# Performance work log

Measured on AMD Instinct MI355X. Metric: run time of the kernel, lower is better.

Reference implementation:

```python
import jax, jax.numpy as jnp
import numpy as np

HOPS = 3  # max_hops; C has HOPS+1 embedding tables


def setup_inputs() -> dict:
    key = jax.random.key(0)
    k1, k2 = jax.random.split(key)
    # story: [memory_len, batch, token_size]
    story = jax.random.randint(k1, (2048, 64, 4), 0, 50000, dtype=jnp.int64)
    # stacked embedding tables C_0..C_3: [hop+1, vocab, embed_dim], N(0, 0.1)
    C = 0.1 * jax.random.normal(k2, (HOPS + 1, 50000, 128), dtype=jnp.float32)
    return {"story": story, "C": C}


def reference(story, C):
    # story: [M, B, T] -> [B, M, T]
    story = jnp.transpose(story, (1, 0, 2))
    B, M, T = story.shape
    D = C.shape[-1]
    # padding_idx=0 semantics: embedding of token 0 is zero (fwd and bwd)
    pad_mask = (story != 0).astype(C.dtype)[..., None]  # [B, M, T, 1]

    u = jnp.zeros((B, D), dtype=C.dtype)
    for hop in range(HOPS):
        # gather + mask + sum over token dim -> memory keys m_A: [B, M, D]
        m_A = jnp.sum(C[hop][story] * pad_mask, axis=2)
        # attention scores over memory slots, softmax along M
        prob = jax.nn.softmax(jnp.einsum('bmd,bd->bm', m_A, u), axis=1)
        # memory values m_C from next-hop table: [B, M, D]
        m_C = jnp.sum(C[hop + 1][story] * pad_mask, axis=2)
        o_k = jnp.einsum('bm,bmd->bd', prob, m_C)
        u = u + o_k
    return u
```

## Files before the change

kernel.cpp:

```cpp
#include <hip/hip_runtime.h>

#define MM 2048
#define BB 64
#define TT 4
#define DD 128
#define VV 50000
#define VPAD 50176
#define NPART 392
#define NATT 512

typedef float f4v __attribute__((ext_vector_type(4)));
typedef short s8v __attribute__((ext_vector_type(8)));

__device__ __forceinline__ unsigned short f2bf(float f) {
    unsigned int u = __float_as_uint(f);
    u = u + 0x7FFFu + ((u >> 16) & 1u);
    return (unsigned short)(u >> 16);
}
__device__ __forceinline__ float bf2f(unsigned short s) {
    return __uint_as_float((unsigned)s << 16);
}
__device__ __forceinline__ unsigned pk2(float lo, float hi) {
    return ((unsigned)f2bf(hi) << 16) | f2bf(lo);
}

__global__ void k_init(float4* __restrict__ p) {
    p[blockIdx.x * 256 + threadIdx.x] = make_float4(0.f, 0.f, 0.f, 0.f);
}

__global__ __launch_bounds__(256) void k_scatter0(const int* __restrict__ st,
                                                  float* __restrict__ W) {
    const int g = blockIdx.x * 256 + threadIdx.x;
    const int b = g & 63;
    const float p = 1.0f / (float)MM;
    const int4 tk = *(const int4*)(st + (size_t)g * 4);
    if (tk.x) atomicAdd(W + (size_t)tk.x * 64 + b, p);
    if (tk.y) atomicAdd(W + (size_t)tk.y * 64 + b, p);
    if (tk.z) atomicAdd(W + (size_t)tk.z * 64 + b, p);
    if (tk.w) atomicAdd(W + (size_t)tk.w * 64 + b, p);
}

__global__ __launch_bounds__(256, 3) void k_gemm_p(const float* __restrict__ Ch,
                                                   const float* __restrict__ u,
                                                   float* __restrict__ P) {
    __shared__ short lds[192 * 136];
    const int t = threadIdx.x;
    const int v0 = blockIdx.x * 128;

#pragma unroll
    for (int i = 0; i < 24; ++i) {
        const int G = i * 256 + t;
        const int row = G >> 5;
        const int c4 = G & 31;
        float4 val;
        if (row < 128) {
            const int v = v0 + row;
            val = (v < VV) ? *(const float4*)(Ch + (size_t)v * DD + c4 * 4)
                           : make_float4(0.f, 0.f, 0.f, 0.f);
        } else {
            val = *(const float4*)(u + (size_t)(row - 128) * DD + c4 * 4);
        }
        const unsigned int lo = ((unsigned int)f2bf(val.y) << 16) | f2bf(val.x);
        const unsigned int hi = ((unsigned int)f2bf(val.w) << 16) | f2bf(val.z);
        *(uint2*)(lds + row * 136 + c4 * 4) = make_uint2(lo, hi);
    }
    __syncthreads();

    const int l = t & 63;
    const int w = t >> 6;
    const int quad = l >> 4;
    const int n16 = l & 15;

    const int ar0 = (32 * w + n16) * 136;
    const int ar1 = (32 * w + 16 + n16) * 136;
    const int br0 = (128 + n16) * 136;
    const int br1 = (144 + n16) * 136;
    const int br2 = (160 + n16) * 136;
    const int br3 = (176 + n16) * 136;

    f4v c00 = {0.f, 0.f, 0.f, 0.f}, c01 = c00, c02 = c00, c03 = c00;
    f4v c10 = c00, c11 = c00, c12 = c00, c13 = c00;

#pragma unroll
    for (int s = 0; s < 4; ++s) {
        const int ko = s * 32 + quad * 8;
        const s8v a0 = *(const s8v*)(lds + ar0 + ko);
        const s8v a1 = *(const s8v*)(lds + ar1 + ko);
        const s8v b0 = *(const s8v*)(lds + br0 + ko);
        const s8v b1 = *(const s8v*)(lds + br1 + ko);
        const s8v b2 = *(const s8v*)(lds + br2 + ko);
        const s8v b3 = *(const s8v*)(lds + br3 + ko);
        c00 = __builtin_amdgcn_mfma_f32_16x16x32_bf16(a0, b0, c00, 0, 0, 0);
        c01 = __builtin_amdgcn_mfma_f32_16x16x32_bf16(a0, b1, c01, 0, 0, 0);
        c02 = __builtin_amdgcn_mfma_f32_16x16x32_bf16(a0, b2, c02, 0, 0, 0);
        c03 = __builtin_amdgcn_mfma_f32_16x16x32_bf16(a0, b3, c03, 0, 0, 0);
        c10 = __builtin_amdgcn_mfma_f32_16x16x32_bf16(a1, b0, c10, 0, 0, 0);
        c11 = __builtin_amdgcn_mfma_f32_16x16x32_bf16(a1, b1, c11, 0, 0, 0);
        c12 = __builtin_amdgcn_mfma_f32_16x16x32_bf16(a1, b2, c12, 0, 0, 0);
        c13 = __builtin_amdgcn_mfma_f32_16x16x32_bf16(a1, b3, c13, 0, 0, 0);
    }

    const int vb0 = v0 + 32 * w + quad * 4;
    const int vb1 = vb0 + 16;
#pragma unroll
    for (int r = 0; r < 4; ++r) {
        float* __restrict__ P0 = P + (size_t)(vb0 + r) * 64 + n16;
        P0[0] = c00[r]; P0[16] = c01[r]; P0[32] = c02[r]; P0[48] = c03[r];
        float* __restrict__ P1 = P + (size_t)(vb1 + r) * 64 + n16;
        P1[0] = c10[r]; P1[16] = c11[r]; P1[32] = c12[r]; P1[48] = c13[r];
    }
}

__global__ __launch_bounds__(256) void k_attn2(const int* __restrict__ st,
                                               const float* __restrict__ P,
                                               float* __restrict__ W,
                                               float* __restrict__ Zp) {
    __shared__ float eb[256];
    const int tid = threadIdx.x;
    const int g = blockIdx.x * 256 + tid;
    const int b = g & 63;

    const int4 tk = *(const int4*)(st + (size_t)g * 4);
    float s = 0.f;
    if (tk.x) s += P[(size_t)tk.x * 64 + b];
    if (tk.y) s += P[(size_t)tk.y * 64 + b];
    if (tk.z) s += P[(size_t)tk.z * 64 + b];
    if (tk.w) s += P[(size_t)tk.w * 64 + b];
    const float e = __expf(s);
    eb[tid] = e;

    if (tk.x) atomicAdd(W + (size_t)tk.x * 64 + b, e);
    if (tk.y) atomicAdd(W + (size_t)tk.y * 64 + b, e);
    if (tk.z) atomicAdd(W + (size_t)tk.z * 64 + b, e);
    if (tk.w) atomicAdd(W + (size_t)tk.w * 64 + b, e);

    __syncthreads();
    if (tid < 64)
        Zp[(size_t)blockIdx.x * 64 + tid] =
            (eb[tid] + eb[tid + 64]) + (eb[tid + 128] + eb[tid + 192]);
}

__global__ __launch_bounds__(256, 3) void k_gemm_o(const float* __restrict__ C2,
                                                   float* __restrict__ W,
                                                   unsigned* __restrict__ upk,
                                                   const int rezero) {
    __shared__ unsigned Wt[64 * 68];
    __shared__ unsigned Ct[128 * 68];
    const int t = threadIdx.x;
    const int vb = blockIdx.x * 128;

#pragma unroll
    for (int i = 0; i < 4; ++i) {
        const int item = i * 256 + t;
        const int q = item & 15;
        const int p = item >> 4;
        float* w0 = W + (size_t)(vb + 2 * p) * 64 + 4 * q;
        float* w1 = W + (size_t)(vb + 2 * p + 1) * 64 + 4 * q;
        const float4 x = *(const float4*)w0;
        const float4 y = *(const float4*)w1;
        if (rezero) {
            *(float4*)w0 = make_float4(0.f, 0.f, 0.f, 0.f);
            *(float4*)w1 = make_float4(0.f, 0.f, 0.f, 0.f);
        }
        Wt[(4 * q + 0) * 68 + p] = pk2(x.x, y.x);
        Wt[(4 * q + 1) * 68 + p] = pk2(x.y, y.y);
        Wt[(4 * q + 2) * 68 + p] = pk2(x.z, y.z);
        Wt[(4 * q + 3) * 68 + p] = pk2(x.w, y.w);
    }
#pragma unroll
    for (int i = 0; i < 8; ++i) {
        const int item = i * 256 + t;
        const int q = item & 31;
        const int p = item >> 5;
        const int v0 = vb + 2 * p;
        const float4 x = (v0 < VV)
            ? *(const float4*)(C2 + (size_t)v0 * DD + 4 * q)
            : make_float4(0.f, 0.f, 0.f, 0.f);
        const float4 y = (v0 + 1 < VV)
            ? *(const float4*)(C2 + (size_t)(v0 + 1) * DD + 4 * q)
            : make_float4(0.f, 0.f, 0.f, 0.f);
        Ct[(4 * q + 0) * 68 + p] = pk2(x.x, y.x);
        Ct[(4 * q + 1) * 68 + p] = pk2(x.y, y.y);
        Ct[(4 * q + 2) * 68 + p] = pk2(x.z, y.z);
        Ct[(4 * q + 3) * 68 + p] = pk2(x.w, y.w);
    }
    __syncthreads();

    const int l = t & 63;
    const int w = t >> 6;
    const int quad = l >> 4;
    const int n16 = l & 15;

    f4v a00 = {0.f, 0.f, 0.f, 0.f}, a01 = a00;
    f4v a10 = a00, a11 = a00, a20 = a00, a21 = a00, a30 = a00, a31 = a00;

#pragma unroll
    for (int ch = 0; ch < 4; ++ch) {
        const int ku = ch * 16 + quad * 4;
        const s8v wa0 = *(const s8v*)&Wt[(0  + n16) * 68 + ku];
        const s8v wa1 = *(const s8v*)&Wt[(16 + n16) * 68 + ku];
        const s8v wa2 = *(const s8v*)&Wt[(32 + n16) * 68 + ku];
        const s8v wa3 = *(const s8v*)&Wt[(48 + n16) * 68 + ku];
        const s8v cb0 = *(const s8v*)&Ct[(w * 32 + n16) * 68 + ku];
        const s8v cb1 = *(const s8v*)&Ct[(w * 32 + 16 + n16) * 68 + ku];
        a00 = __builtin_amdgcn_mfma_f32_16x16x32_bf16(wa0, cb0, a00, 0, 0, 0);
        a01 = __builtin_amdgcn_mfma_f32_16x16x32_bf16(wa0, cb1, a01, 0, 0, 0);
        a10 = __builtin_amdgcn_mfma_f32_16x16x32_bf16(wa1, cb0, a10, 0, 0, 0);
        a11 = __builtin_amdgcn_mfma_f32_16x16x32_bf16(wa1, cb1, a11, 0, 0, 0);
        a20 = __builtin_amdgcn_mfma_f32_16x16x32_bf16(wa2, cb0, a20, 0, 0, 0);
        a21 = __builtin_amdgcn_mfma_f32_16x16x32_bf16(wa2, cb1, a21, 0, 0, 0);
        a30 = __builtin_amdgcn_mfma_f32_16x16x32_bf16(wa3, cb0, a30, 0, 0, 0);
        a31 = __builtin_amdgcn_mfma_f32_16x16x32_bf16(wa3, cb1, a31, 0, 0, 0);
    }

    unsigned* __restrict__ up = upk + (size_t)blockIdx.x * (BB * 64);
    const int wi = w * 16 + n16;
#pragma unroll
    for (int r = 0; r < 4; ++r) {
        const int br = quad * 4 + r;
        up[(br +  0) * 64 + wi] = pk2(a00[r], a01[r]);
        up[(br + 16) * 64 + wi] = pk2(a10[r], a11[r]);
        up[(br + 32) * 64 + wi] = pk2(a20[r], a21[r]);
        up[(br + 48) * 64 + wi] = pk2(a30[r], a31[r]);
    }
}

__device__ __forceinline__ float zwave(const float* __restrict__ Zp, int b, int tid) {
    const int lane = tid & 63;
    float z = 0.f;
#pragma unroll
    for (int i = 0; i < 8; ++i)
        z += Zp[(size_t)(lane * 8 + i) * 64 + b];
#pragma unroll
    for (int off = 32; off; off >>= 1) z += __shfl_xor(z, off, 64);
    return z;
}

__global__ __launch_bounds__(256) void k_reduce_a(const unsigned* __restrict__ upk,
                                                  float* __restrict__ u) {
    const int jc = blockIdx.x & 15;
    const int kc = blockIdx.x >> 4;
    const int jw = jc * 256 + threadIdx.x;
    const unsigned* __restrict__ p = upk + (size_t)kc * 49 * (BB * 64) + jw;
    float lo = 0.f, hi = 0.f;
#pragma unroll 7
    for (int k = 0; k < 49; ++k) {
        const unsigned w = p[(size_t)k * (BB * 64)];
        lo += bf2f((unsigned short)w);
        hi += bf2f((unsigned short)(w >> 16));
    }
    const int b = jw >> 6, wi = jw & 63;
    const int d0 = (wi >> 4) * 32 + (wi & 15);
    atomicAdd(u + b * DD + d0, lo);
    atomicAdd(u + b * DD + d0 + 16, hi);
}

__global__ __launch_bounds__(256) void k_reduce_az(const unsigned* __restrict__ upk,
                                                   const float* __restrict__ Zp,
                                                   float* __restrict__ u) {
    const int jc = blockIdx.x & 15;
    const int kc = blockIdx.x >> 4;
    const int tid = threadIdx.x;
    const int jw = jc * 256 + tid;
    const int b = jw >> 6;
    const float rz = 1.f / zwave(Zp, b, tid);
    const unsigned* __restrict__ p = upk + (size_t)kc * 49 * (BB * 64) + jw;
    float lo = 0.f, hi = 0.f;
#pragma unroll 7
    for (int k = 0; k < 49; ++k) {
        const unsigned w = p[(size_t)k * (BB * 64)];
        lo += bf2f((unsigned short)w);
        hi += bf2f((unsigned short)(w >> 16));
    }
    const int wi = jw & 63;
    const int d0 = (wi >> 4) * 32 + (wi & 15);
    atomicAdd(u + b * DD + d0, lo * rz);
    atomicAdd(u + b * DD + d0 + 16, hi * rz);
}

__global__ __launch_bounds__(256) void k_reduce_finz(const unsigned* __restrict__ upk,
                                                     const float* __restrict__ Zp,
                                                     const float* __restrict__ u,
                                                     float* __restrict__ out) {
    const int tid = threadIdx.x;
    const int jw = blockIdx.x * 256 + tid;
    const int b = jw >> 6;
    const float rz = 1.f / zwave(Zp, b, tid);
    const unsigned* __restrict__ p = upk + jw;
    float lo = 0.f, hi = 0.f;
#pragma unroll 8
    for (int k = 0; k < NPART; ++k) {
        const unsigned w = p[(size_t)k * (BB * 64)];
        lo += bf2f((unsigned short)w);
        hi += bf2f((unsigned short)(w >> 16));
    }
    const int wi = jw & 63;
    const int d0 = (wi >> 4) * 32 + (wi & 15);
    out[b * DD + d0]      = u[b * DD + d0]      + lo * rz;
    out[b * DD + d0 + 16] = u[b * DD + d0 + 16] + hi * rz;
}

extern "C" void kernel_launch(void* const* d_in, const int* in_sizes, int n_in,
                              void* d_out, int out_size, void* d_ws, size_t ws_size,
                              hipStream_t stream) {
    const int* st = (const int*)d_in[0];
    const float* C = (const float*)d_in[1];

    float* u  = (float*)d_ws;
    float* W  = u + BB * DD;
    float* P  = W + (size_t)VPAD * BB;
    unsigned* upk = (unsigned*)(P + (size_t)VPAD * BB);
    float* Zp = (float*)(upk + (size_t)NPART * BB * 64);

    k_init<<<(BB * DD + VPAD * BB) / 1024, 256, 0, stream>>>((float4*)u);

    k_scatter0<<<(MM * BB) / 256, 256, 0, stream>>>(st, W);
    k_gemm_o<<<VPAD / 128, 256, 0, stream>>>(C + (size_t)1 * VV * DD, W, upk, 1);
    k_reduce_a<<<128, 256, 0, stream>>>(upk, u);

    k_gemm_p<<<VPAD / 128, 256, 0, stream>>>(C + (size_t)1 * VV * DD, u, P);
    k_attn2<<<NATT, 256, 0, stream>>>(st, P, W, Zp);
    k_gemm_o<<<VPAD / 128, 256, 0, stream>>>(C + (size_t)2 * VV * DD, W, upk, 1);
    k_reduce_az<<<128, 256, 0, stream>>>(upk, Zp, u);

    k_gemm_p<<<VPAD / 128, 256, 0, stream>>>(C + (size_t)2 * VV * DD, u, P);
    k_attn2<<<NATT, 256, 0, stream>>>(st, P, W, Zp);
    k_gemm_o<<<VPAD / 128, 256, 0, stream>>>(C + (size_t)3 * VV * DD, W, upk, 0);
    k_reduce_finz<<<16, 256, 0, stream>>>(upk, Zp, u, (float*)d_out);
}
```

Before: 312.6 us.

## Store projection scores in bf16 and use one thread per token in scatter/attention

The per-vocab score table P is now written as bf16 by the projection GEMM and read as bf16 in the attention kernel, halving its footprint and traffic. The scatter and attention kernels now use one thread per token instead of per (slot,batch). Token scores are combined with lane shuffles, and the partial-sum buffer grows to match the larger grid. The goal is more memory-level parallelism for the random gathers and atomics. The cost is bf16 rounding of the scores before exp, plus a longer Z reduction loop.

```diff
diff --git a/kernel.cpp b/kernel.cpp
--- a/kernel.cpp
+++ b/kernel.cpp
@@ -7,7 +7,7 @@
 #define VV 50000
 #define VPAD 50176
 #define NPART 392
-#define NATT 512
+#define NATT 2048
 
 typedef float f4v __attribute__((ext_vector_type(4)));
 typedef short s8v __attribute__((ext_vector_type(8)));
@@ -30,19 +30,15 @@
 
 __global__ __launch_bounds__(256) void k_scatter0(const int* __restrict__ st,
                                                   float* __restrict__ W) {
-    const int g = blockIdx.x * 256 + threadIdx.x;
-    const int b = g & 63;
-    const float p = 1.0f / (float)MM;
-    const int4 tk = *(const int4*)(st + (size_t)g * 4);
-    if (tk.x) atomicAdd(W + (size_t)tk.x * 64 + b, p);
-    if (tk.y) atomicAdd(W + (size_t)tk.y * 64 + b, p);
-    if (tk.z) atomicAdd(W + (size_t)tk.z * 64 + b, p);
-    if (tk.w) atomicAdd(W + (size_t)tk.w * 64 + b, p);
+    const int g4 = blockIdx.x * 256 + threadIdx.x;
+    const int b = (g4 >> 2) & 63;
+    const int tok = st[g4];
+    if (tok) atomicAdd(W + (size_t)tok * 64 + b, 1.0f / (float)MM);
 }
 
 __global__ __launch_bounds__(256, 3) void k_gemm_p(const float* __restrict__ Ch,
                                                    const float* __restrict__ u,
-                                                   float* __restrict__ P) {
+                                                   unsigned short* __restrict__ P16) {
     __shared__ short lds[192 * 136];
     const int t = threadIdx.x;
     const int v0 = blockIdx.x * 128;
@@ -104,40 +100,36 @@
     const int vb1 = vb0 + 16;
 #pragma unroll
     for (int r = 0; r < 4; ++r) {
-        float* __restrict__ P0 = P + (size_t)(vb0 + r) * 64 + n16;
-        P0[0] = c00[r]; P0[16] = c01[r]; P0[32] = c02[r]; P0[48] = c03[r];
-        float* __restrict__ P1 = P + (size_t)(vb1 + r) * 64 + n16;
-        P1[0] = c10[r]; P1[16] = c11[r]; P1[32] = c12[r]; P1[48] = c13[r];
+        unsigned short* __restrict__ P0 = P16 + (size_t)(vb0 + r) * 64 + n16;
+        P0[0]  = f2bf(c00[r]); P0[16] = f2bf(c01[r]);
+        P0[32] = f2bf(c02[r]); P0[48] = f2bf(c03[r]);
+        unsigned short* __restrict__ P1 = P16 + (size_t)(vb1 + r) * 64 + n16;
+        P1[0]  = f2bf(c10[r]); P1[16] = f2bf(c11[r]);
+        P1[32] = f2bf(c12[r]); P1[48] = f2bf(c13[r]);
     }
 }
 
 __global__ __launch_bounds__(256) void k_attn2(const int* __restrict__ st,
-                                               const float* __restrict__ P,
+                                               const unsigned short* __restrict__ P16,
                                                float* __restrict__ W,
                                                float* __restrict__ Zp) {
-    __shared__ float eb[256];
+    __shared__ float eb[64];
     const int tid = threadIdx.x;
-    const int g = blockIdx.x * 256 + tid;
-    const int b = g & 63;
-
-    const int4 tk = *(const int4*)(st + (size_t)g * 4);
-    float s = 0.f;
-    if (tk.x) s += P[(size_t)tk.x * 64 + b];
-    if (tk.y) s += P[(size_t)tk.y * 64 + b];
-    if (tk.z) s += P[(size_t)tk.z * 64 + b];
-    if (tk.w) s += P[(size_t)tk.w * 64 + b];
-    const float e = __expf(s);
-    eb[tid] = e;
-
-    if (tk.x) atomicAdd(W + (size_t)tk.x * 64 + b, e);
-    if (tk.y) atomicAdd(W + (size_t)tk.y * 64 + b, e);
-    if (tk.z) atomicAdd(W + (size_t)tk.z * 64 + b, e);
-    if (tk.w) atomicAdd(W + (size_t)tk.w * 64 + b, e);
-
+    const int g4 = blockIdx.x * 256 + tid;
+    const int b = (g4 >> 2) & 63;
+
+    const int tok = st[g4];
+    float v = 0.f;
+    if (tok) v = bf2f(P16[(size_t)tok * 64 + b]);
+    v += __shfl_xor(v, 1, 64);
+    v += __shfl_xor(v, 2, 64);
+    const float e = __expf(v);
+
+    if (tok) atomicAdd(W + (size_t)tok * 64 + b, e);
+
+    if ((tid & 3) == 0) eb[tid >> 2] = e;
     __syncthreads();
-    if (tid < 64)
-        Zp[(size_t)blockIdx.x * 64 + tid] =
-            (eb[tid] + eb[tid + 64]) + (eb[tid + 128] + eb[tid + 192]);
+    if (tid < 64) Zp[(size_t)blockIdx.x * 64 + tid] = eb[tid];
 }
 
 __global__ __launch_bounds__(256, 3) void k_gemm_o(const float* __restrict__ C2,
@@ -229,8 +221,8 @@
     const int lane = tid & 63;
     float z = 0.f;
 #pragma unroll
-    for (int i = 0; i < 8; ++i)
-        z += Zp[(size_t)(lane * 8 + i) * 64 + b];
+    for (int i = 0; i < 32; ++i)
+        z += Zp[(size_t)(lane * 32 + i) * 64 + b];
 #pragma unroll
     for (int off = 32; off; off >>= 1) z += __shfl_xor(z, off, 64);
     return z;
@@ -308,23 +300,23 @@
 
     float* u  = (float*)d_ws;
     float* W  = u + BB * DD;
-    float* P  = W + (size_t)VPAD * BB;
-    unsigned* upk = (unsigned*)(P + (size_t)VPAD * BB);
+    unsigned short* P16 = (unsigned short*)(W + (size_t)VPAD * BB);
+    unsigned* upk = (unsigned*)(P16 + (size_t)VPAD * BB);
     float* Zp = (float*)(upk + (size_t)NPART * BB * 64);
 
     k_init<<<(BB * DD + VPAD * BB) / 1024, 256, 0, stream>>>((float4*)u);
 
-    k_scatter0<<<(MM * BB) / 256, 256, 0, stream>>>(st, W);
+    k_scatter0<<<(MM * BB * TT) / 256, 256, 0, stream>>>(st, W);
     k_gemm_o<<<VPAD / 128, 256, 0, stream>>>(C + (size_t)1 * VV * DD, W, upk, 1);
     k_reduce_a<<<128, 256, 0, stream>>>(upk, u);
 
-    k_gemm_p<<<VPAD / 128, 256, 0, stream>>>(C + (size_t)1 * VV * DD, u, P);
-    k_attn2<<<NATT, 256, 0, stream>>>(st, P, W, Zp);
+    k_gemm_p<<<VPAD / 128, 256, 0, stream>>>(C + (size_t)1 * VV * DD, u, P16);
+    k_attn2<<<NATT, 256, 0, stream>>>(st, P16, W, Zp);
     k_gemm_o<<<VPAD / 128, 256, 0, stream>>>(C + (size_t)2 * VV * DD, W, upk, 1);
     k_reduce_az<<<128, 256, 0, stream>>>(upk, Zp, u);
 
-    k_gemm_p<<<VPAD / 128, 256, 0, stream>>>(C + (size_t)2 * VV * DD, u, P);
-    k_attn2<<<NATT, 256, 0, stream>>>(st, P, W, Zp);
+    k_gemm_p<<<VPAD / 128, 256, 0, stream>>>(C + (size_t)2 * VV * DD, u, P16);
+    k_attn2<<<NATT, 256, 0, stream>>>(st, P16, W, Zp);
     k_gemm_o<<<VPAD / 128, 256, 0, stream>>>(C + (size_t)3 * VV * DD, W, upk, 0);
     k_reduce_finz<<<16, 256, 0, stream>>>(upk, Zp, u, (float*)d_out);
 }
```

Result: no change. 313.6 us (+0.3%).
